# Kernel optimization log

Measured on AMD Instinct MI355X. Metric: run time of the kernel, lower is better.

Reference implementation:

```python
import jax, jax.numpy as jnp
import numpy as np
from jax.scipy.special import logsumexp

HEAD = 12
EPS = 1.0


def _sinkhorn(dots):
    # dots: [b, h, n, n]. Faithful to the torch code: eps=1, max_iter=3,
    # update order u, v, u (the err<1e-6 early-break never triggers for
    # unconverged random-scale inputs, so we unroll the 3 iterations).
    C = -dots
    b, h, n, m = C.shape
    log_mu = -jnp.log(jnp.asarray(n, dtype=C.dtype))  # log(1/n)
    log_nu = -jnp.log(jnp.asarray(m, dtype=C.dtype))
    u = jnp.zeros((b, h, n), dtype=C.dtype)
    v = jnp.zeros((b, h, m), dtype=C.dtype)

    def M(u, v):
        # (-C + u_i + v_j) / eps
        return (-C + u[..., :, None] + v[..., None, :]) / EPS

    # i = 0: row update
    u = EPS * (log_mu - logsumexp(M(u, v), axis=-1)) + u
    # i = 1: column update (logsumexp over transpose == axis=-2)
    v = EPS * (log_nu - logsumexp(M(u, v), axis=-2)) + v
    # i = 2: row update
    u = EPS * (log_mu - logsumexp(M(u, v), axis=-1)) + u
    return jnp.exp(M(u, v))


def setup_inputs() -> dict:
    key = jax.random.key(0)
    ks = jax.random.split(key, 6)
    b, n, f = 8, 1024, 768
    x = jax.random.normal(ks[0], (b, n, f), dtype=jnp.float32)
    s = 1.0 / np.sqrt(f)
    Wq = jax.random.normal(ks[1], (f, f), dtype=jnp.float32) * s
    Wk = jax.random.normal(ks[2], (f, f), dtype=jnp.float32) * s
    Wv = jax.random.normal(ks[3], (f, f), dtype=jnp.float32) * s
    Wo = jax.random.normal(ks[4], (f, f), dtype=jnp.float32) * s
    bo = jax.random.normal(ks[5], (f,), dtype=jnp.float32) * 0.01
    return {"x": x, "Wq": Wq, "Wk": Wk, "Wv": Wv, "Wo": Wo, "bo": bo}


def reference(x, Wq, Wk, Wv, Wo, bo):
    b, n, f = x.shape
    h = HEAD
    d = f // h
    scale = d ** (-0.5)
    # nn.Linear: y = x @ W.T
    q = (x @ Wq.T).reshape(b, n, h, d).transpose(0, 2, 1, 3)  # [b,h,n,d]
    k = (x @ Wk.T).reshape(b, n, h, d).transpose(0, 2, 1, 3)
    v = (x @ Wv.T).reshape(b, n, h, d).transpose(0, 2, 1, 3)
    dots = jnp.einsum("bhid,bhjd->bhij", q, k) * scale  # [b,h,n,n]
    attn = _sinkhorn(dots)
    out = jnp.einsum("bhij,bhjd->bhid", attn, v)
    out = out.transpose(0, 2, 1, 3).reshape(b, n, f)
    return out @ Wo.T + bo
```

## Files before the change

kernel.cpp:

```cpp
#include <hip/hip_runtime.h>

#define DEV __device__ __forceinline__

typedef __attribute__((ext_vector_type(4))) float f32x4;
typedef __attribute__((ext_vector_type(16))) float f32x16;
typedef __attribute__((ext_vector_type(8))) short bf16x8;
typedef __attribute__((ext_vector_type(4))) short bf16x4;

DEV short f2bf(float f) {
    union { float f; unsigned u; } v; v.f = f;
    unsigned r = (v.u + 0x7fffu + ((v.u >> 16) & 1u)) >> 16;
    return (short)r;
}

#ifndef __has_builtin
#define __has_builtin(x) 0
#endif
#if __has_builtin(__builtin_amdgcn_cvt_pk_bf16_f32)
DEV unsigned pkbf(float a, float b) {
    auto r = __builtin_amdgcn_cvt_pk_bf16_f32(a, b);
    union { __typeof__(r) v; unsigned u; } u; u.v = r; return u.u;
}
#else
DEV unsigned pkbf(float a, float b) {
    return (unsigned)(unsigned short)f2bf(a) | ((unsigned)(unsigned short)f2bf(b) << 16);
}
#endif

DEV void gl_lds16(const void* g, void* l) {
    __builtin_amdgcn_global_load_lds(
        (__attribute__((address_space(1))) void*)(g),
        (__attribute__((address_space(3))) void*)(l), 16, 0, 0);
}

template <int ITERS>
DEV void stage_tile(const short* g, int ldg, short* lds, int t) {
    const int w = t >> 6;
#pragma unroll
    for (int it = 0; it < ITERS; ++it) {
        int row = it * 32 + (t >> 3);
        int cx = (t & 7) ^ ((t >> 3) & 7);
        gl_lds16(g + row * ldg + cx * 8, (char*)lds + it * 4096 + (w << 10));
    }
}

DEV bf16x8 ldfrag(const short* lds, int r, int kc) {
    return *(const bf16x8*)(lds + r * 64 + ((kc ^ (r & 7)) << 3));
}

__global__ void cvt_all(const float* __restrict__ x,
                        const float* __restrict__ wq, const float* __restrict__ wk,
                        const float* __restrict__ wv, const float* __restrict__ wo,
                        short* __restrict__ xb,
                        short* __restrict__ wqb, short* __restrict__ wkb,
                        short* __restrict__ wvb, short* __restrict__ wob) {
    int b = blockIdx.x;
    const float* s; short* d; int i;
    if (b < 6144) {
        s = x; d = xb; i = b * 256 + threadIdx.x;
    } else {
        int r = b - 6144;
        int wi = r / 576, rem = r - wi * 576;
        s = (wi == 0) ? wq : (wi == 1) ? wk : (wi == 2) ? wv : wo;
        d = (wi == 0) ? wqb : (wi == 1) ? wkb : (wi == 2) ? wvb : wob;
        i = rem * 256 + threadIdx.x;
    }
    float4 v = ((const float4*)s)[i];
    short4 o;
    o.x = f2bf(v.x); o.y = f2bf(v.y); o.z = f2bf(v.z); o.w = f2bf(v.w);
    ((short4*)d)[i] = o;
}

#define TSTRIDE 136
__global__ __launch_bounds__(256, 4) void proj_gemm(
    const short* __restrict__ xb,
    const short* __restrict__ wq, const short* __restrict__ wk, const short* __restrict__ wv,
    short* __restrict__ Qg, short* __restrict__ Kg, short* __restrict__ Vtg)
{
    __shared__ __align__(16) char smem[128 * TSTRIDE * 2];
    short* At = (short*)smem;
    short* Bt = (short*)(smem + 128 * 64 * 2);
    short* Ct = (short*)smem;
    const int t = threadIdx.x;
    const int z = blockIdx.z;
    const int row0 = blockIdx.x * 128, col0 = blockIdx.y * 128;
    const int lane = t & 63, w = t >> 6;
    const int l31 = lane & 31, lh = lane >> 5;
    const int wm = w >> 1, wn = w & 1;
    const short* W = (z == 0) ? wq : (z == 1) ? wk : wv;

    f32x16 acc[2][2];
#pragma unroll
    for (int i = 0; i < 2; ++i)
#pragma unroll
        for (int j = 0; j < 2; ++j) acc[i][j] = (f32x16)(0.f);

    for (int k0 = 0; k0 < 768; k0 += 64) {
        __syncthreads();
        stage_tile<4>(xb + (size_t)row0 * 768 + k0, 768, At, t);
        stage_tile<4>(W + (size_t)col0 * 768 + k0, 768, Bt, t);
        __syncthreads();
#pragma unroll
        for (int s = 0; s < 4; ++s) {
            bf16x8 af[2], bfr[2];
#pragma unroll
            for (int tm = 0; tm < 2; ++tm) af[tm] = ldfrag(At, wm * 64 + tm * 32 + l31, s * 2 + lh);
#pragma unroll
            for (int tn = 0; tn < 2; ++tn) bfr[tn] = ldfrag(Bt, wn * 64 + tn * 32 + l31, s * 2 + lh);
#pragma unroll
            for (int tm = 0; tm < 2; ++tm)
#pragma unroll
                for (int tn = 0; tn < 2; ++tn)
                    acc[tm][tn] = __builtin_amdgcn_mfma_f32_32x32x16_bf16(af[tm], bfr[tn], acc[tm][tn], 0, 0, 0);
        }
    }

    __syncthreads();
    if (z == 2) {
#pragma unroll
        for (int tm = 0; tm < 2; ++tm)
#pragma unroll
            for (int tn = 0; tn < 2; ++tn) {
                int ddl = wn * 64 + tn * 32 + l31;
#pragma unroll
                for (int g = 0; g < 4; ++g) {
                    int rrl = wm * 64 + tm * 32 + 8 * g + 4 * lh;
                    int j6 = rrl & 63;
                    int pp = (rrl & ~63) | (j6 & 32) | ((j6 & 12) << 1) | ((j6 & 16) >> 2);
                    short4 v4;
                    v4.x = f2bf(acc[tm][tn][4 * g + 0]);
                    v4.y = f2bf(acc[tm][tn][4 * g + 1]);
                    v4.z = f2bf(acc[tm][tn][4 * g + 2]);
                    v4.w = f2bf(acc[tm][tn][4 * g + 3]);
                    *(short4*)(Ct + ddl * TSTRIDE + pp) = v4;
                }
            }
    } else {
        const float sc = (z == 0) ? 0.125f * 1.4426950408889634f : 1.0f;
#pragma unroll
        for (int tm = 0; tm < 2; ++tm)
#pragma unroll
            for (int tn = 0; tn < 2; ++tn) {
                int ddl = wn * 64 + tn * 32 + l31;
#pragma unroll
                for (int reg = 0; reg < 16; ++reg) {
                    int rrl = wm * 64 + tm * 32 + (reg & 3) + 8 * (reg >> 2) + 4 * lh;
                    Ct[rrl * TSTRIDE + ddl] = f2bf(acc[tm][tn][reg] * sc);
                }
            }
    }
    __syncthreads();

    const int bb = row0 >> 10;
#pragma unroll
    for (int it = 0; it < 8; ++it) {
        int row = it * 16 + (t >> 4);
        int ck = t & 15;
        bf16x8 v = *(const bf16x8*)(Ct + row * TSTRIDE + ck * 8);
        if (z == 2) {
            int gdd = col0 + row;
            int head = bb * 12 + (gdd >> 6);
            *(bf16x8*)(Vtg + ((size_t)head * 64 + (gdd & 63)) * 1024 + (row0 & 1023) + ck * 8) = v;
        } else {
            int rr = (row0 & 1023) + row;
            int gc = col0 + ck * 8;
            int head = bb * 12 + (gc >> 6);
            short* dst = (z == 0) ? Qg : Kg;
            *(bf16x8*)(dst + ((size_t)head * 1024 + rr) * 64 + (gc & 63)) = v;
        }
    }
}

__global__ __launch_bounds__(256, 5) void lse_pass(
    const short* __restrict__ Aall, const short* __restrict__ Ball,
    const float* __restrict__ bias, float* __restrict__ outv,
    float bias_sign, float out_sign)
{
    __shared__ __align__(16) short At[64 * 64];
    __shared__ __align__(16) short Bt[128 * 64];
    __shared__ __align__(16) float biasl[1024];
    const int t = threadIdx.x;
    const int head = blockIdx.x % 96;
    const int r0 = (blockIdx.x / 96) * 64;
    const int lane = t & 63, w = t >> 6, quad = lane >> 4, c = lane & 15;
    const short* A = Aall + (size_t)head * 65536;
    const short* B = Ball + (size_t)head * 65536;

    stage_tile<2>(A + r0 * 64, 64, At, t);
    if (bias) {
        float4 v = ((const float4*)(bias + (size_t)head * 1024))[t];
        v.x *= bias_sign; v.y *= bias_sign; v.z *= bias_sign; v.w *= bias_sign;
        ((float4*)biasl)[t] = v;
    } else ((float4*)biasl)[t] = make_float4(0.f, 0.f, 0.f, 0.f);

    float lsum = 0.f;

    for (int j0 = 0; j0 < 1024; j0 += 128) {
        __syncthreads();
        stage_tile<4>(B + j0 * 64, 64, Bt, t);
        __syncthreads();
        f32x4 sacc[8];
#pragma unroll
        for (int fm = 0; fm < 8; ++fm) {
            float4 b4 = *(const float4*)(biasl + j0 + fm * 16 + quad * 4);
            sacc[fm] = (f32x4){b4.x, b4.y, b4.z, b4.w};
        }
#pragma unroll
        for (int ks = 0; ks < 2; ++ks) {
            bf16x8 af[8], bfr;
#pragma unroll
            for (int fm = 0; fm < 8; ++fm) af[fm] = ldfrag(Bt, fm * 16 + c, ks * 4 + quad);
            bfr = ldfrag(At, w * 16 + c, ks * 4 + quad);
#pragma unroll
            for (int fm = 0; fm < 8; ++fm)
                sacc[fm] = __builtin_amdgcn_mfma_f32_16x16x32_bf16(af[fm], bfr, sacc[fm], 0, 0, 0);
        }
#pragma unroll
        for (int fm = 0; fm < 8; ++fm) {
            float p0 = __builtin_amdgcn_exp2f(sacc[fm][0]);
            float p1 = __builtin_amdgcn_exp2f(sacc[fm][1]);
            float p2 = __builtin_amdgcn_exp2f(sacc[fm][2]);
            float p3 = __builtin_amdgcn_exp2f(sacc[fm][3]);
            lsum += (p0 + p1) + (p2 + p3);
        }
    }

    lsum += __shfl_xor(lsum, 16);
    lsum += __shfl_xor(lsum, 32);
    if (quad == 0)
        outv[(size_t)head * 1024 + r0 + w * 16 + c] =
            out_sign * __builtin_amdgcn_logf(lsum);
}

__global__ __launch_bounds__(256, 4) void flash_pass(
    const short* __restrict__ Qall, const short* __restrict__ Kall,
    const short* __restrict__ Vtall, const float* __restrict__ v1,
    short* __restrict__ ctx)
{
    __shared__ __align__(16) short Qt[128 * 64];
    __shared__ __align__(16) short Kt[64 * 64];
    __shared__ __align__(16) short Vtl[64 * 64];
    __shared__ __align__(16) float v1l[1024];
    const int t = threadIdx.x;
    const int head = blockIdx.x % 96;
    const int r0 = (blockIdx.x / 96) * 128;
    const int lane = t & 63, w = t >> 6, quad = lane >> 4, c = lane & 15;
    const short* Q = Qall + (size_t)head * 65536;
    const short* K = Kall + (size_t)head * 65536;
    const short* Vt = Vtall + (size_t)head * 65536;

    stage_tile<4>(Q + r0 * 64, 64, Qt, t);
    ((float4*)v1l)[t] = ((const float4*)(v1 + (size_t)head * 1024))[t];

    float lsum[2] = {0.f, 0.f};
    f32x4 oacc[4][2];
#pragma unroll
    for (int md = 0; md < 4; ++md)
#pragma unroll
        for (int ni = 0; ni < 2; ++ni) oacc[md][ni] = (f32x4){0.f, 0.f, 0.f, 0.f};

    for (int j0 = 0; j0 < 1024; j0 += 64) {
        __syncthreads();
        stage_tile<2>(K + j0 * 64, 64, Kt, t);
        stage_tile<2>(Vt + j0, 1024, Vtl, t);
        __syncthreads();
        f32x4 sacc[4][2];
#pragma unroll
        for (int fm = 0; fm < 4; ++fm) {
            float4 b4 = *(const float4*)(v1l + j0 + fm * 16 + quad * 4);
#pragma unroll
            for (int fn = 0; fn < 2; ++fn) sacc[fm][fn] = (f32x4){b4.x, b4.y, b4.z, b4.w};
        }
#pragma unroll
        for (int ks = 0; ks < 2; ++ks) {
            bf16x8 af[4], bfr[2];
#pragma unroll
            for (int fm = 0; fm < 4; ++fm) af[fm] = ldfrag(Kt, fm * 16 + c, ks * 4 + quad);
#pragma unroll
            for (int fn = 0; fn < 2; ++fn) bfr[fn] = ldfrag(Qt, w * 32 + fn * 16 + c, ks * 4 + quad);
#pragma unroll
            for (int fm = 0; fm < 4; ++fm)
#pragma unroll
                for (int fn = 0; fn < 2; ++fn)
                    sacc[fm][fn] = __builtin_amdgcn_mfma_f32_16x16x32_bf16(af[fm], bfr[fn], sacc[fm][fn], 0, 0, 0);
        }
        unsigned pk[4][2][2];
#pragma unroll
        for (int fm = 0; fm < 4; ++fm)
#pragma unroll
            for (int fn = 0; fn < 2; ++fn) {
                float p0 = __builtin_amdgcn_exp2f(sacc[fm][fn][0]);
                float p1 = __builtin_amdgcn_exp2f(sacc[fm][fn][1]);
                float p2 = __builtin_amdgcn_exp2f(sacc[fm][fn][2]);
                float p3 = __builtin_amdgcn_exp2f(sacc[fm][fn][3]);
                lsum[fn] += (p0 + p1) + (p2 + p3);
                pk[fm][fn][0] = pkbf(p0, p1);
                pk[fm][fn][1] = pkbf(p2, p3);
            }
#pragma unroll
        for (int ks = 0; ks < 2; ++ks) {
            bf16x8 vaf[4];
#pragma unroll
            for (int md = 0; md < 4; ++md) vaf[md] = ldfrag(Vtl, md * 16 + c, ks * 4 + quad);
#pragma unroll
            for (int ni = 0; ni < 2; ++ni) {
                union { bf16x8 v8; unsigned u4[4]; } b;
                b.u4[0] = pk[2 * ks + 0][ni][0];
                b.u4[1] = pk[2 * ks + 0][ni][1];
                b.u4[2] = pk[2 * ks + 1][ni][0];
                b.u4[3] = pk[2 * ks + 1][ni][1];
#pragma unroll
                for (int md = 0; md < 4; ++md)
                    oacc[md][ni] = __builtin_amdgcn_mfma_f32_16x16x32_bf16(vaf[md], b.v8, oacc[md][ni], 0, 0, 0);
            }
        }
    }

#pragma unroll
    for (int fn = 0; fn < 2; ++fn) {
        float s = lsum[fn];
        s += __shfl_xor(s, 16); s += __shfl_xor(s, 32);
        lsum[fn] = s;
    }
    const int bb = head / 12, hh = head % 12;
#pragma unroll
    for (int ni = 0; ni < 2; ++ni) {
        float nrm = __builtin_amdgcn_rcpf(1024.f * lsum[ni]);
        int rr = r0 + w * 32 + ni * 16 + c;
#pragma unroll
        for (int md = 0; md < 4; ++md) {
            short4 v4;
            v4.x = f2bf(oacc[md][ni][0] * nrm);
            v4.y = f2bf(oacc[md][ni][1] * nrm);
            v4.z = f2bf(oacc[md][ni][2] * nrm);
            v4.w = f2bf(oacc[md][ni][3] * nrm);
            *(short4*)(ctx + ((size_t)(bb * 1024 + rr)) * 768 + hh * 64 + md * 16 + quad * 4) = v4;
        }
    }
}

__global__ __launch_bounds__(256, 4) void out_gemm(
    const short* __restrict__ ctxb, const short* __restrict__ wo,
    const float* __restrict__ bo, float* __restrict__ out)
{
    __shared__ __align__(16) short At[128 * 64];
    __shared__ __align__(16) short Bt[128 * 64];
    const int t = threadIdx.x;
    const int row0 = blockIdx.x * 128, col0 = blockIdx.y * 128;
    const int lane = t & 63, w = t >> 6;
    const int l31 = lane & 31, lh = lane >> 5;
    const int wm = w >> 1, wn = w & 1;

    f32x16 acc[2][2];
#pragma unroll
    for (int i = 0; i < 2; ++i)
#pragma unroll
        for (int j = 0; j < 2; ++j) acc[i][j] = (f32x16)(0.f);

    for (int k0 = 0; k0 < 768; k0 += 64) {
        __syncthreads();
        stage_tile<4>(ctxb + (size_t)row0 * 768 + k0, 768, At, t);
        stage_tile<4>(wo + (size_t)col0 * 768 + k0, 768, Bt, t);
        __syncthreads();
#pragma unroll
        for (int s = 0; s < 4; ++s) {
            bf16x8 af[2], bfr[2];
#pragma unroll
            for (int tm = 0; tm < 2; ++tm) af[tm] = ldfrag(At, wm * 64 + tm * 32 + l31, s * 2 + lh);
#pragma unroll
            for (int tn = 0; tn < 2; ++tn) bfr[tn] = ldfrag(Bt, wn * 64 + tn * 32 + l31, s * 2 + lh);
#pragma unroll
            for (int tm = 0; tm < 2; ++tm)
#pragma unroll
                for (int tn = 0; tn < 2; ++tn)
                    acc[tm][tn] = __builtin_amdgcn_mfma_f32_32x32x16_bf16(af[tm], bfr[tn], acc[tm][tn], 0, 0, 0);
        }
    }
#pragma unroll
    for (int tm = 0; tm < 2; ++tm)
#pragma unroll
        for (int tn = 0; tn < 2; ++tn) {
            int gc = col0 + wn * 64 + tn * 32 + l31;
            float b = bo[gc];
#pragma unroll
            for (int reg = 0; reg < 16; ++reg) {
                int gr = row0 + wm * 64 + tm * 32 + (reg & 3) + 8 * (reg >> 2) + 4 * lh;
                out[(size_t)gr * 768 + gc] = acc[tm][tn][reg] + b;
            }
        }
}

extern "C" void kernel_launch(void* const* d_in, const int* in_sizes, int n_in,
                              void* d_out, int out_size, void* d_ws, size_t ws_size,
                              hipStream_t stream) {
    const float* x  = (const float*)d_in[0];
    const float* Wq = (const float*)d_in[1];
    const float* Wk = (const float*)d_in[2];
    const float* Wv = (const float*)d_in[3];
    const float* Wo = (const float*)d_in[4];
    const float* bo = (const float*)d_in[5];
    float* out = (float*)d_out;

    char* p = (char*)d_ws;
    short* xb  = (short*)p; p += (size_t)8192 * 768 * 2;
    short* wqb = (short*)p; p += (size_t)768 * 768 * 2;
    short* wkb = (short*)p; p += (size_t)768 * 768 * 2;
    short* wvb = (short*)p; p += (size_t)768 * 768 * 2;
    short* wob = (short*)p; p += (size_t)768 * 768 * 2;
    short* Qg  = (short*)p; p += (size_t)96 * 1024 * 64 * 2;
    short* Kg  = (short*)p; p += (size_t)96 * 1024 * 64 * 2;
    short* Vtg = (short*)p; p += (size_t)96 * 1024 * 64 * 2;
    float* r1  = (float*)p; p += (size_t)96 * 1024 * 4;
    float* v1  = (float*)p; p += (size_t)96 * 1024 * 4;
    short* ctx = (short*)p; p += (size_t)8192 * 768 * 2;

    cvt_all<<<6144 + 4 * 576, 256, 0, stream>>>(x, Wq, Wk, Wv, Wo, xb, wqb, wkb, wvb, wob);

    proj_gemm<<<dim3(64, 6, 3), 256, 0, stream>>>(xb, wqb, wkb, wvb, Qg, Kg, Vtg);

    lse_pass<<<1536, 256, 0, stream>>>(Qg, Kg, nullptr, r1, 0.f, 1.f);
    lse_pass<<<1536, 256, 0, stream>>>(Kg, Qg, r1, v1, -1.f, -1.f);

    flash_pass<<<768, 256, 0, stream>>>(Qg, Kg, Vtg, v1, ctx);

    out_gemm<<<dim3(64, 6), 256, 0, stream>>>(ctx, wob, bo, out);
}
```

Baseline: 218.5 us.

## Double-buffer LDS tiles in GEMM, LSE and flash kernels to overlap loads

Adds ping-pong LDS buffers to proj_gemm, out_gemm, lse_pass and flash_pass. The next K/V/B tile is staged while the current one is consumed, so each iteration needs one barrier instead of two. Loop-invariant Q/A fragments are now loaded into registers once, before the loop. The cost is doubled LDS use and lower launch-bounds occupancy (2-3 blocks instead of 4-5), and stage_tile appears synchronous, so real overlap depends on how the compiler schedules the loads.

```diff
diff --git a/kernel.cpp b/kernel.cpp
--- a/kernel.cpp
+++ b/kernel.cpp
@@ -72,15 +72,17 @@
 }
 
 #define TSTRIDE 136
-__global__ __launch_bounds__(256, 4) void proj_gemm(
+__global__ __launch_bounds__(256, 2) void proj_gemm(
     const short* __restrict__ xb,
     const short* __restrict__ wq, const short* __restrict__ wk, const short* __restrict__ wv,
     short* __restrict__ Qg, short* __restrict__ Kg, short* __restrict__ Vtg)
 {
-    __shared__ __align__(16) char smem[128 * TSTRIDE * 2];
-    short* At = (short*)smem;
-    short* Bt = (short*)(smem + 128 * 64 * 2);
-    short* Ct = (short*)smem;
+    __shared__ __align__(16) char smem[65536];
+    short* const A0 = (short*)smem;
+    short* const B0 = (short*)(smem + 16384);
+    short* const A1 = (short*)(smem + 32768);
+    short* const B1 = (short*)(smem + 49152);
+    short* const Ct = (short*)smem;
     const int t = threadIdx.x;
     const int z = blockIdx.z;
     const int row0 = blockIdx.x * 128, col0 = blockIdx.y * 128;
@@ -88,6 +90,8 @@
     const int l31 = lane & 31, lh = lane >> 5;
     const int wm = w >> 1, wn = w & 1;
     const short* W = (z == 0) ? wq : (z == 1) ? wk : wv;
+    const short* Asrc = xb + (size_t)row0 * 768;
+    const short* Bsrc = W + (size_t)col0 * 768;
 
     f32x16 acc[2][2];
 #pragma unroll
@@ -95,11 +99,16 @@
 #pragma unroll
         for (int j = 0; j < 2; ++j) acc[i][j] = (f32x16)(0.f);
 
-    for (int k0 = 0; k0 < 768; k0 += 64) {
-        __syncthreads();
-        stage_tile<4>(xb + (size_t)row0 * 768 + k0, 768, At, t);
-        stage_tile<4>(W + (size_t)col0 * 768 + k0, 768, Bt, t);
-        __syncthreads();
+    stage_tile<4>(Asrc, 768, A0, t);
+    stage_tile<4>(Bsrc, 768, B0, t);
+    __syncthreads();
+    for (int k = 0; k < 12; ++k) {
+        if (k < 11) {
+            stage_tile<4>(Asrc + (k + 1) * 64, 768, (k & 1) ? A0 : A1, t);
+            stage_tile<4>(Bsrc + (k + 1) * 64, 768, (k & 1) ? B0 : B1, t);
+        }
+        const short* At = (k & 1) ? A1 : A0;
+        const short* Bt = (k & 1) ? B1 : B0;
 #pragma unroll
         for (int s = 0; s < 4; ++s) {
             bf16x8 af[2], bfr[2];
@@ -113,9 +122,9 @@
                 for (int tn = 0; tn < 2; ++tn)
                     acc[tm][tn] = __builtin_amdgcn_mfma_f32_32x32x16_bf16(af[tm], bfr[tn], acc[tm][tn], 0, 0, 0);
         }
-    }
-
-    __syncthreads();
+        __syncthreads();
+    }
+
     if (z == 2) {
 #pragma unroll
         for (int tm = 0; tm < 2; ++tm)
@@ -171,13 +180,13 @@
     }
 }
 
-__global__ __launch_bounds__(256, 5) void lse_pass(
+__global__ __launch_bounds__(256, 3) void lse_pass(
     const short* __restrict__ Aall, const short* __restrict__ Ball,
     const float* __restrict__ bias, float* __restrict__ outv,
     float bias_sign, float out_sign)
 {
     __shared__ __align__(16) short At[64 * 64];
-    __shared__ __align__(16) short Bt[128 * 64];
+    __shared__ __align__(16) short Bbuf[2 * 128 * 64];
     __shared__ __align__(16) float biasl[1024];
     const int t = threadIdx.x;
     const int head = blockIdx.x % 96;
@@ -187,18 +196,24 @@
     const short* B = Ball + (size_t)head * 65536;
 
     stage_tile<2>(A + r0 * 64, 64, At, t);
+    stage_tile<4>(B, 64, Bbuf, t);
     if (bias) {
         float4 v = ((const float4*)(bias + (size_t)head * 1024))[t];
         v.x *= bias_sign; v.y *= bias_sign; v.z *= bias_sign; v.w *= bias_sign;
         ((float4*)biasl)[t] = v;
     } else ((float4*)biasl)[t] = make_float4(0.f, 0.f, 0.f, 0.f);
+    __syncthreads();
+
+    bf16x8 bfr[2];
+#pragma unroll
+    for (int ks = 0; ks < 2; ++ks) bfr[ks] = ldfrag(At, w * 16 + c, ks * 4 + quad);
 
     float lsum = 0.f;
 
-    for (int j0 = 0; j0 < 1024; j0 += 128) {
-        __syncthreads();
-        stage_tile<4>(B + j0 * 64, 64, Bt, t);
-        __syncthreads();
+    for (int j = 0; j < 8; ++j) {
+        if (j < 7) stage_tile<4>(B + (j + 1) * 128 * 64, 64, Bbuf + ((j + 1) & 1) * 128 * 64, t);
+        const short* Bt = Bbuf + (j & 1) * 128 * 64;
+        const int j0 = j * 128;
         f32x4 sacc[8];
 #pragma unroll
         for (int fm = 0; fm < 8; ++fm) {
@@ -207,13 +222,12 @@
         }
 #pragma unroll
         for (int ks = 0; ks < 2; ++ks) {
-            bf16x8 af[8], bfr;
+            bf16x8 af[8];
 #pragma unroll
             for (int fm = 0; fm < 8; ++fm) af[fm] = ldfrag(Bt, fm * 16 + c, ks * 4 + quad);
-            bfr = ldfrag(At, w * 16 + c, ks * 4 + quad);
 #pragma unroll
             for (int fm = 0; fm < 8; ++fm)
-                sacc[fm] = __builtin_amdgcn_mfma_f32_16x16x32_bf16(af[fm], bfr, sacc[fm], 0, 0, 0);
+                sacc[fm] = __builtin_amdgcn_mfma_f32_16x16x32_bf16(af[fm], bfr[ks], sacc[fm], 0, 0, 0);
         }
 #pragma unroll
         for (int fm = 0; fm < 8; ++fm) {
@@ -223,6 +237,7 @@
             float p3 = __builtin_amdgcn_exp2f(sacc[fm][3]);
             lsum += (p0 + p1) + (p2 + p3);
         }
+        __syncthreads();
     }
 
     lsum += __shfl_xor(lsum, 16);
@@ -232,14 +247,14 @@
             out_sign * __builtin_amdgcn_logf(lsum);
 }
 
-__global__ __launch_bounds__(256, 4) void flash_pass(
+__global__ __launch_bounds__(256, 3) void flash_pass(
     const short* __restrict__ Qall, const short* __restrict__ Kall,
     const short* __restrict__ Vtall, const float* __restrict__ v1,
     short* __restrict__ ctx)
 {
     __shared__ __align__(16) short Qt[128 * 64];
-    __shared__ __align__(16) short Kt[64 * 64];
-    __shared__ __align__(16) short Vtl[64 * 64];
+    __shared__ __align__(16) short Kbuf[2 * 64 * 64];
+    __shared__ __align__(16) short Vbuf[2 * 64 * 64];
     __shared__ __align__(16) float v1l[1024];
     const int t = threadIdx.x;
     const int head = blockIdx.x % 96;
@@ -250,7 +265,17 @@
     const short* Vt = Vtall + (size_t)head * 65536;
 
     stage_tile<4>(Q + r0 * 64, 64, Qt, t);
+    stage_tile<2>(K, 64, Kbuf, t);
+    stage_tile<2>(Vt, 1024, Vbuf, t);
     ((float4*)v1l)[t] = ((const float4*)(v1 + (size_t)head * 1024))[t];
+    __syncthreads();
+
+    bf16x8 qfr[2][2];
+#pragma unroll
+    for (int fn = 0; fn < 2; ++fn)
+#pragma unroll
+        for (int ks = 0; ks < 2; ++ks)
+            qfr[fn][ks] = ldfrag(Qt, w * 32 + fn * 16 + c, ks * 4 + quad);
 
     float lsum[2] = {0.f, 0.f};
     f32x4 oacc[4][2];
@@ -259,11 +284,14 @@
 #pragma unroll
         for (int ni = 0; ni < 2; ++ni) oacc[md][ni] = (f32x4){0.f, 0.f, 0.f, 0.f};
 
-    for (int j0 = 0; j0 < 1024; j0 += 64) {
-        __syncthreads();
-        stage_tile<2>(K + j0 * 64, 64, Kt, t);
-        stage_tile<2>(Vt + j0, 1024, Vtl, t);
-        __syncthreads();
+    for (int j = 0; j < 16; ++j) {
+        if (j < 15) {
+            stage_tile<2>(K + (j + 1) * 64 * 64, 64, Kbuf + ((j + 1) & 1) * 64 * 64, t);
+            stage_tile<2>(Vt + (j + 1) * 64, 1024, Vbuf + ((j + 1) & 1) * 64 * 64, t);
+        }
+        const short* Kt = Kbuf + (j & 1) * 64 * 64;
+        const short* Vtl = Vbuf + (j & 1) * 64 * 64;
+        const int j0 = j * 64;
         f32x4 sacc[4][2];
 #pragma unroll
         for (int fm = 0; fm < 4; ++fm) {
@@ -273,16 +301,14 @@
         }
 #pragma unroll
         for (int ks = 0; ks < 2; ++ks) {
-            bf16x8 af[4], bfr[2];
+            bf16x8 af[4];
 #pragma unroll
             for (int fm = 0; fm < 4; ++fm) af[fm] = ldfrag(Kt, fm * 16 + c, ks * 4 + quad);
 #pragma unroll
-            for (int fn = 0; fn < 2; ++fn) bfr[fn] = ldfrag(Qt, w * 32 + fn * 16 + c, ks * 4 + quad);
-#pragma unroll
             for (int fm = 0; fm < 4; ++fm)
 #pragma unroll
                 for (int fn = 0; fn < 2; ++fn)
-                    sacc[fm][fn] = __builtin_amdgcn_mfma_f32_16x16x32_bf16(af[fm], bfr[fn], sacc[fm][fn], 0, 0, 0);
+                    sacc[fm][fn] = __builtin_amdgcn_mfma_f32_16x16x32_bf16(af[fm], qfr[fn][ks], sacc[fm][fn], 0, 0, 0);
         }
         unsigned pk[4][2][2];
 #pragma unroll
@@ -314,6 +340,7 @@
                     oacc[md][ni] = __builtin_amdgcn_mfma_f32_16x16x32_bf16(vaf[md], b.v8, oacc[md][ni], 0, 0, 0);
             }
         }
+        __syncthreads();
     }
 
 #pragma unroll
@@ -339,17 +366,22 @@
     }
 }
 
-__global__ __launch_bounds__(256, 4) void out_gemm(
+__global__ __launch_bounds__(256, 2) void out_gemm(
     const short* __restrict__ ctxb, const short* __restrict__ wo,
     const float* __restrict__ bo, float* __restrict__ out)
 {
-    __shared__ __align__(16) short At[128 * 64];
-    __shared__ __align__(16) short Bt[128 * 64];
+    __shared__ __align__(16) char smem[65536];
+    short* const A0 = (short*)smem;
+    short* const B0 = (short*)(smem + 16384);
+    short* const A1 = (short*)(smem + 32768);
+    short* const B1 = (short*)(smem + 49152);
     const int t = threadIdx.x;
     const int row0 = blockIdx.x * 128, col0 = blockIdx.y * 128;
     const int lane = t & 63, w = t >> 6;
     const int l31 = lane & 31, lh = lane >> 5;
     const int wm = w >> 1, wn = w & 1;
+    const short* Asrc = ctxb + (size_t)row0 * 768;
+    const short* Bsrc = wo + (size_t)col0 * 768;
 
     f32x16 acc[2][2];
 #pragma unroll
@@ -357,11 +389,16 @@
 #pragma unroll
         for (int j = 0; j < 2; ++j) acc[i][j] = (f32x16)(0.f);
 
-    for (int k0 = 0; k0 < 768; k0 += 64) {
-        __syncthreads();
-        stage_tile<4>(ctxb + (size_t)row0 * 768 + k0, 768, At, t);
-        stage_tile<4>(wo + (size_t)col0 * 768 + k0, 768, Bt, t);
-        __syncthreads();
+    stage_tile<4>(Asrc, 768, A0, t);
+    stage_tile<4>(Bsrc, 768, B0, t);
+    __syncthreads();
+    for (int k = 0; k < 12; ++k) {
+        if (k < 11) {
+            stage_tile<4>(Asrc + (k + 1) * 64, 768, (k & 1) ? A0 : A1, t);
+            stage_tile<4>(Bsrc + (k + 1) * 64, 768, (k & 1) ? B0 : B1, t);
+        }
+        const short* At = (k & 1) ? A1 : A0;
+        const short* Bt = (k & 1) ? B1 : B0;
 #pragma unroll
         for (int s = 0; s < 4; ++s) {
             bf16x8 af[2], bfr[2];
@@ -375,6 +412,7 @@
                 for (int tn = 0; tn < 2; ++tn)
                     acc[tm][tn] = __builtin_amdgcn_mfma_f32_32x32x16_bf16(af[tm], bfr[tn], acc[tm][tn], 0, 0, 0);
         }
+        __syncthreads();
     }
 #pragma unroll
     for (int tm = 0; tm < 2; ++tm)
```

Measured after the change: 227.8 us. +4.3%, slower.

## Fuse Q/K/V projections per block sharing the x tile; hoist loop-invariant fragments

Applied to the files above, without the earlier changes.

The projection GEMM now computes Q, K and V for a 128x64 output tile in one block, staging the x tile once and reusing it across three weight tiles. Previously the x tile was reloaded for each of the three projections. Each block now holds three accumulator sets, and the launch bound drops to 3 waves per SIMD. In lse_pass and flash_pass, the query-side MFMA fragments are loaded from shared memory once instead of on every key tile.

```diff
diff --git a/kernel.cpp b/kernel.cpp
--- a/kernel.cpp
+++ b/kernel.cpp
@@ -5,7 +5,6 @@
 typedef __attribute__((ext_vector_type(4))) float f32x4;
 typedef __attribute__((ext_vector_type(16))) float f32x16;
 typedef __attribute__((ext_vector_type(8))) short bf16x8;
-typedef __attribute__((ext_vector_type(4))) short bf16x4;
 
 DEV short f2bf(float f) {
     union { float f; unsigned u; } v; v.f = f;
@@ -72,101 +71,109 @@
 }
 
 #define TSTRIDE 136
-__global__ __launch_bounds__(256, 4) void proj_gemm(
+__global__ __launch_bounds__(256, 3) void proj_gemm(
     const short* __restrict__ xb,
     const short* __restrict__ wq, const short* __restrict__ wk, const short* __restrict__ wv,
     short* __restrict__ Qg, short* __restrict__ Kg, short* __restrict__ Vtg)
 {
-    __shared__ __align__(16) char smem[128 * TSTRIDE * 2];
-    short* At = (short*)smem;
-    short* Bt = (short*)(smem + 128 * 64 * 2);
-    short* Ct = (short*)smem;
+    __shared__ __align__(16) char smem[40960];
+    short* const At = (short*)smem;
+    short* const Bq = (short*)(smem + 16384);
+    short* const Bk = (short*)(smem + 24576);
+    short* const Bv = (short*)(smem + 32768);
+    short* const Ct = (short*)smem;
     const int t = threadIdx.x;
-    const int z = blockIdx.z;
-    const int row0 = blockIdx.x * 128, col0 = blockIdx.y * 128;
+    const int row0 = blockIdx.x * 128, col0 = blockIdx.y * 64;
     const int lane = t & 63, w = t >> 6;
     const int l31 = lane & 31, lh = lane >> 5;
     const int wm = w >> 1, wn = w & 1;
-    const short* W = (z == 0) ? wq : (z == 1) ? wk : wv;
-
-    f32x16 acc[2][2];
-#pragma unroll
-    for (int i = 0; i < 2; ++i)
-#pragma unroll
-        for (int j = 0; j < 2; ++j) acc[i][j] = (f32x16)(0.f);
-
-    for (int k0 = 0; k0 < 768; k0 += 64) {
-        __syncthreads();
-        stage_tile<4>(xb + (size_t)row0 * 768 + k0, 768, At, t);
-        stage_tile<4>(W + (size_t)col0 * 768 + k0, 768, Bt, t);
+
+    f32x16 acc[3][2];
+#pragma unroll
+    for (int z = 0; z < 3; ++z)
+#pragma unroll
+        for (int tm = 0; tm < 2; ++tm) acc[z][tm] = (f32x16)(0.f);
+
+    const short* Asrc = xb + (size_t)row0 * 768;
+    const short* Qs = wq + (size_t)col0 * 768;
+    const short* Ks = wk + (size_t)col0 * 768;
+    const short* Vs = wv + (size_t)col0 * 768;
+
+    for (int k = 0; k < 12; ++k) {
+        __syncthreads();
+        stage_tile<4>(Asrc + k * 64, 768, At, t);
+        stage_tile<2>(Qs + k * 64, 768, Bq, t);
+        stage_tile<2>(Ks + k * 64, 768, Bk, t);
+        stage_tile<2>(Vs + k * 64, 768, Bv, t);
         __syncthreads();
 #pragma unroll
         for (int s = 0; s < 4; ++s) {
-            bf16x8 af[2], bfr[2];
+            bf16x8 af[2];
 #pragma unroll
             for (int tm = 0; tm < 2; ++tm) af[tm] = ldfrag(At, wm * 64 + tm * 32 + l31, s * 2 + lh);
-#pragma unroll
-            for (int tn = 0; tn < 2; ++tn) bfr[tn] = ldfrag(Bt, wn * 64 + tn * 32 + l31, s * 2 + lh);
-#pragma unroll
-            for (int tm = 0; tm < 2; ++tm)
-#pragma unroll
-                for (int tn = 0; tn < 2; ++tn)
-                    acc[tm][tn] = __builtin_amdgcn_mfma_f32_32x32x16_bf16(af[tm], bfr[tn], acc[tm][tn], 0, 0, 0);
-        }
-    }
-
+            bf16x8 b0 = ldfrag(Bq, wn * 32 + l31, s * 2 + lh);
+            bf16x8 b1 = ldfrag(Bk, wn * 32 + l31, s * 2 + lh);
+            bf16x8 b2 = ldfrag(Bv, wn * 32 + l31, s * 2 + lh);
+#pragma unroll
+            for (int tm = 0; tm < 2; ++tm) {
+                acc[0][tm] = __builtin_amdgcn_mfma_f32_32x32x16_bf16(af[tm], b0, acc[0][tm], 0, 0, 0);
+                acc[1][tm] = __builtin_amdgcn_mfma_f32_32x32x16_bf16(af[tm], b1, acc[1][tm], 0, 0, 0);
+                acc[2][tm] = __builtin_amdgcn_mfma_f32_32x32x16_bf16(af[tm], b2, acc[2][tm], 0, 0, 0);
+            }
+        }
+    }
     __syncthreads();
-    if (z == 2) {
+
+    const int bb = row0 >> 10;
+    const int head = bb * 12 + (col0 >> 6);
+
+#pragma unroll
+    for (int z = 0; z < 2; ++z) {
+        const float sc = (z == 0) ? 0.125f * 1.4426950408889634f : 1.0f;
+        const int ddl = wn * 32 + l31;
 #pragma unroll
         for (int tm = 0; tm < 2; ++tm)
 #pragma unroll
-            for (int tn = 0; tn < 2; ++tn) {
-                int ddl = wn * 64 + tn * 32 + l31;
-#pragma unroll
-                for (int g = 0; g < 4; ++g) {
-                    int rrl = wm * 64 + tm * 32 + 8 * g + 4 * lh;
-                    int j6 = rrl & 63;
-                    int pp = (rrl & ~63) | (j6 & 32) | ((j6 & 12) << 1) | ((j6 & 16) >> 2);
-                    short4 v4;
-                    v4.x = f2bf(acc[tm][tn][4 * g + 0]);
-                    v4.y = f2bf(acc[tm][tn][4 * g + 1]);
-                    v4.z = f2bf(acc[tm][tn][4 * g + 2]);
-                    v4.w = f2bf(acc[tm][tn][4 * g + 3]);
-                    *(short4*)(Ct + ddl * TSTRIDE + pp) = v4;
-                }
-            }
-    } else {
-        const float sc = (z == 0) ? 0.125f * 1.4426950408889634f : 1.0f;
+            for (int reg = 0; reg < 16; ++reg) {
+                int rrl = wm * 64 + tm * 32 + (reg & 3) + 8 * (reg >> 2) + 4 * lh;
+                Ct[rrl * TSTRIDE + ddl] = f2bf(acc[z][tm][reg] * sc);
+            }
+        __syncthreads();
+        short* dst = (z == 0) ? Qg : Kg;
+#pragma unroll
+        for (int it = 0; it < 4; ++it) {
+            int row = it * 32 + (t >> 3);
+            int ck = t & 7;
+            bf16x8 v = *(const bf16x8*)(Ct + row * TSTRIDE + ck * 8);
+            int rr = (row0 & 1023) + row;
+            *(bf16x8*)(dst + ((size_t)head * 1024 + rr) * 64 + ck * 8) = v;
+        }
+        __syncthreads();
+    }
+
+    {
+        const int ddl = wn * 32 + l31;
 #pragma unroll
         for (int tm = 0; tm < 2; ++tm)
 #pragma unroll
-            for (int tn = 0; tn < 2; ++tn) {
-                int ddl = wn * 64 + tn * 32 + l31;
-#pragma unroll
-                for (int reg = 0; reg < 16; ++reg) {
-                    int rrl = wm * 64 + tm * 32 + (reg & 3) + 8 * (reg >> 2) + 4 * lh;
-                    Ct[rrl * TSTRIDE + ddl] = f2bf(acc[tm][tn][reg] * sc);
-                }
-            }
-    }
-    __syncthreads();
-
-    const int bb = row0 >> 10;
-#pragma unroll
-    for (int it = 0; it < 8; ++it) {
-        int row = it * 16 + (t >> 4);
-        int ck = t & 15;
-        bf16x8 v = *(const bf16x8*)(Ct + row * TSTRIDE + ck * 8);
-        if (z == 2) {
-            int gdd = col0 + row;
-            int head = bb * 12 + (gdd >> 6);
-            *(bf16x8*)(Vtg + ((size_t)head * 64 + (gdd & 63)) * 1024 + (row0 & 1023) + ck * 8) = v;
-        } else {
-            int rr = (row0 & 1023) + row;
-            int gc = col0 + ck * 8;
-            int head = bb * 12 + (gc >> 6);
-            short* dst = (z == 0) ? Qg : Kg;
-            *(bf16x8*)(dst + ((size_t)head * 1024 + rr) * 64 + (gc & 63)) = v;
+            for (int g = 0; g < 4; ++g) {
+                int rrl = wm * 64 + tm * 32 + 8 * g + 4 * lh;
+                int j6 = rrl & 63;
+                int pp = (rrl & ~63) | (j6 & 32) | ((j6 & 12) << 1) | ((j6 & 16) >> 2);
+                short4 v4;
+                v4.x = f2bf(acc[2][tm][4 * g + 0]);
+                v4.y = f2bf(acc[2][tm][4 * g + 1]);
+                v4.z = f2bf(acc[2][tm][4 * g + 2]);
+                v4.w = f2bf(acc[2][tm][4 * g + 3]);
+                *(short4*)(Ct + ddl * TSTRIDE + pp) = v4;
+            }
+        __syncthreads();
+#pragma unroll
+        for (int it = 0; it < 4; ++it) {
+            int row = it * 16 + (t >> 4);
+            int ck = t & 15;
+            bf16x8 v = *(const bf16x8*)(Ct + row * TSTRIDE + ck * 8);
+            *(bf16x8*)(Vtg + ((size_t)head * 64 + row) * 1024 + (row0 & 1023) + ck * 8) = v;
         }
     }
 }
@@ -194,11 +201,18 @@
     } else ((float4*)biasl)[t] = make_float4(0.f, 0.f, 0.f, 0.f);
 
     float lsum = 0.f;
+    bf16x8 bfr[2];
+    bool first = true;
 
     for (int j0 = 0; j0 < 1024; j0 += 128) {
         __syncthreads();
         stage_tile<4>(B + j0 * 64, 64, Bt, t);
         __syncthreads();
+        if (first) {
+#pragma unroll
+            for (int ks = 0; ks < 2; ++ks) bfr[ks] = ldfrag(At, w * 16 + c, ks * 4 + quad);
+            first = false;
+        }
         f32x4 sacc[8];
 #pragma unroll
         for (int fm = 0; fm < 8; ++fm) {
@@ -207,13 +221,12 @@
         }
 #pragma unroll
         for (int ks = 0; ks < 2; ++ks) {
-            bf16x8 af[8], bfr;
+            bf16x8 af[8];
 #pragma unroll
             for (int fm = 0; fm < 8; ++fm) af[fm] = ldfrag(Bt, fm * 16 + c, ks * 4 + quad);
-            bfr = ldfrag(At, w * 16 + c, ks * 4 + quad);
 #pragma unroll
             for (int fm = 0; fm < 8; ++fm)
-                sacc[fm] = __builtin_amdgcn_mfma_f32_16x16x32_bf16(af[fm], bfr, sacc[fm], 0, 0, 0);
+                sacc[fm] = __builtin_amdgcn_mfma_f32_16x16x32_bf16(af[fm], bfr[ks], sacc[fm], 0, 0, 0);
         }
 #pragma unroll
         for (int fm = 0; fm < 8; ++fm) {
@@ -259,11 +272,22 @@
 #pragma unroll
         for (int ni = 0; ni < 2; ++ni) oacc[md][ni] = (f32x4){0.f, 0.f, 0.f, 0.f};
 
+    bf16x8 qfr[2][2];
+    bool first = true;
+
     for (int j0 = 0; j0 < 1024; j0 += 64) {
         __syncthreads();
         stage_tile<2>(K + j0 * 64, 64, Kt, t);
         stage_tile<2>(Vt + j0, 1024, Vtl, t);
         __syncthreads();
+        if (first) {
+#pragma unroll
+            for (int fn = 0; fn < 2; ++fn)
+#pragma unroll
+                for (int ks = 0; ks < 2; ++ks)
+                    qfr[fn][ks] = ldfrag(Qt, w * 32 + fn * 16 + c, ks * 4 + quad);
+            first = false;
+        }
         f32x4 sacc[4][2];
 #pragma unroll
         for (int fm = 0; fm < 4; ++fm) {
@@ -273,16 +297,14 @@
         }
 #pragma unroll
         for (int ks = 0; ks < 2; ++ks) {
-            bf16x8 af[4], bfr[2];
+            bf16x8 af[4];
 #pragma unroll
             for (int fm = 0; fm < 4; ++fm) af[fm] = ldfrag(Kt, fm * 16 + c, ks * 4 + quad);
 #pragma unroll
-            for (int fn = 0; fn < 2; ++fn) bfr[fn] = ldfrag(Qt, w * 32 + fn * 16 + c, ks * 4 + quad);
-#pragma unroll
             for (int fm = 0; fm < 4; ++fm)
 #pragma unroll
                 for (int fn = 0; fn < 2; ++fn)
-                    sacc[fm][fn] = __builtin_amdgcn_mfma_f32_16x16x32_bf16(af[fm], bfr[fn], sacc[fm][fn], 0, 0, 0);
+                    sacc[fm][fn] = __builtin_amdgcn_mfma_f32_16x16x32_bf16(af[fm], qfr[fn][ks], sacc[fm][fn], 0, 0, 0);
         }
         unsigned pk[4][2][2];
 #pragma unroll
@@ -416,7 +438,7 @@
 
     cvt_all<<<6144 + 4 * 576, 256, 0, stream>>>(x, Wq, Wk, Wv, Wo, xb, wqb, wkb, wvb, wob);
 
-    proj_gemm<<<dim3(64, 6, 3), 256, 0, stream>>>(xb, wqb, wkb, wvb, Qg, Kg, Vtg);
+    proj_gemm<<<dim3(64, 12), 256, 0, stream>>>(xb, wqb, wkb, wvb, Qg, Kg, Vtg);
 
     lse_pass<<<1536, 256, 0, stream>>>(Qg, Kg, nullptr, r1, 0.f, 1.f);
     lse_pass<<<1536, 256, 0, stream>>>(Kg, Qg, r1, v1, -1.f, -1.f);
```

Result: slower. 224.6 us (+2.8%).
